# Kernel tuning notes

Hardware: AMD Instinct MI355X
Metric: run time of the kernel (lower is better)

## Reference

```python
import jax, jax.numpy as jnp
import numpy as np

C = 512   # in_channels
N = 256   # spatial side (H == W required by the bmm structure)


def setup_inputs() -> dict:
    key = jax.random.key(0)
    kx, kf, kg, kh = jax.random.split(key, 4)
    scale = 1.0 / np.sqrt(C)  # spectral-normalized 1x1 conv weights have ~unit spectral norm
    x = jax.random.normal(kx, (C, N, N), dtype=jnp.float32)
    Wf = jax.random.normal(kf, (C, C), dtype=jnp.float32) * scale  # 1x1 conv kernel squeezed
    Wg = jax.random.normal(kg, (C, C), dtype=jnp.float32) * scale
    Wh = jax.random.normal(kh, (C, C), dtype=jnp.float32) * scale
    return {"x": x, "Wf": Wf, "Wg": Wg, "Wh": Wh}


def reference(x, Wf, Wg, Wh):
    # 1x1 convs (no bias) == channel-mixing matmuls: out[c,h,w] = sum_k W[c,k] x[k,h,w]
    f = jnp.einsum('ck,khw->chw', Wf, x)
    g = jnp.einsum('ck,khw->chw', Wg, x)
    h = jnp.einsum('ck,khw->chw', Wh, x)
    # torch.bmm(f, g): per-channel HxW @ HxW matmul -> [C, N, N]
    scores = jnp.einsum('cik,ckj->cij', f, g)
    # nn.Softmax(dim=1) on [C, N, N] -> softmax over the row axis (axis=1)
    attn_map = jax.nn.softmax(scores, axis=1)
    # torch.bmm(h, attn_map) -> [C, N, N]
    attn = jnp.einsum('cik,ckj->cij', h, attn_map)
    return x + attn
```

## Files before the change

### kernel.cpp

```cpp
#include <hip/hip_runtime.h>

typedef unsigned short u16;
typedef unsigned int   u32;
typedef __attribute__((ext_vector_type(8))) _Float16 half8;
typedef __attribute__((ext_vector_type(4))) float f32x4;
typedef __attribute__((ext_vector_type(2))) float f32x2;
typedef __attribute__((ext_vector_type(4))) u32   u32x4;
typedef __attribute__((ext_vector_type(4))) unsigned short u16x4;

#define MFMAH __builtin_amdgcn_mfma_f32_16x16x32_f16

__device__ u16 W16[786432];

__device__ __forceinline__ u16 f2h(float f) {
  _Float16 h = (_Float16)f;
  union { _Float16 hh; u16 u; } cv; cv.hh = h; return cv.u;
}
__device__ __forceinline__ u32 pkh(float a, float b) {
  return (u32)f2h(a) | ((u32)f2h(b) << 16);
}
__device__ __forceinline__ void gload16(const void* g, void* l) {
  __builtin_amdgcn_global_load_lds(
      (const __attribute__((address_space(1))) void*)g,
      (__attribute__((address_space(3))) void*)l, 16, 0, 0);
}

__global__ __launch_bounds__(256)
void prep_w(const float* __restrict__ Wf, const float* __restrict__ Wg,
            const float* __restrict__ Wh)
{
  const int r = blockIdx.x;
  const int k = threadIdx.x * 2;
  const float* src = (r < 512) ? (Wf + (size_t)r * 512)
                   : (r < 1024) ? (Wg + (size_t)(r - 512) * 512)
                                : (Wh + (size_t)(r - 1024) * 512);
  f32x2 v = *(const f32x2*)(src + k);
  *(u32*)(W16 + (size_t)r * 512 + k) = pkh(v[0], v[1]);
}

__global__ __launch_bounds__(256)
void prep_x(const float* __restrict__ x, u16* __restrict__ x16)
{
  __shared__ float tile[64 * 256];
  const int bk = blockIdx.x & 7, bn = blockIdx.x >> 3;
  const int t = threadIdx.x;
  const int cw = (t & 63) * 4, r0 = (t >> 6) * 16;
#pragma unroll
  for (int it = 0; it < 16; ++it) {
    const int r = r0 + it;
    *(f32x4*)&tile[r * 256 + cw] =
        *(const f32x4*)(x + (size_t)(bk * 64 + r) * 65536 + (size_t)bn * 256 + cw);
  }
  __syncthreads();
  u32 w[32];
#pragma unroll
  for (int q = 0; q < 32; ++q)
    w[q] = pkh(tile[(2 * q) * 256 + t], tile[(2 * q + 1) * 256 + t]);
  const size_t ob = (size_t)(bn * 256 + t) * 512 + bk * 64;
#pragma unroll
  for (int c4 = 0; c4 < 8; ++c4)
    *(u32x4*)(x16 + ob + c4 * 8) = (u32x4){w[4*c4], w[4*c4+1], w[4*c4+2], w[4*c4+3]};
}

__global__ __launch_bounds__(512, 4)
void conv_fgh(const u16* __restrict__ x16, u16* __restrict__ fb,
              u16* __restrict__ gTb, u16* __restrict__ hb)
{
  __shared__ u16 sA[8192], sB[4096];
  const int bid = blockIdx.x;
  const int xcd = bid & 7, idx = bid >> 3;
  const int tn = xcd * 64 + idx / 6;
  const int tm2 = idx % 6;
  const bool gmode = (tm2 >= 2) && (tm2 < 4);
  const int t = threadIdx.x, lane = t & 63, wid = t >> 6;
  const int wr = wid >> 1, wc = wid & 1, lr = lane & 15, lq = lane >> 4;

  const int ar0 = t >> 2, ar1 = 128 + (t >> 2);
  const int aks0 = (((t & 3) ^ ((ar0 >> 1) & 3)) << 3);
  const int aks1 = (((t & 3) ^ ((ar1 >> 1) & 3)) << 3);
  const int garA0 = tm2 * 256 + ar0, garA1 = tm2 * 256 + ar1;
  const int br = t >> 2;
  const int bks = (((t & 3) ^ ((br >> 1) & 3)) << 3);
  const int bxr = gmode ? ((((tn & 1) << 7) + br) * 256 + (tn >> 1)) : (tn * 128 + br);

  int offA[4], offB[4];
#pragma unroll
  for (int mi = 0; mi < 4; ++mi) {
    const int rowA = wr * 64 + mi * 16 + lr;
    offA[mi] = rowA * 32 + ((lq ^ ((rowA >> 1) & 3)) << 3);
  }
#pragma unroll
  for (int ni = 0; ni < 4; ++ni) {
    const int rowB = wc * 64 + ni * 16 + lr;
    offB[ni] = rowB * 32 + ((lq ^ ((rowB >> 1) & 3)) << 3);
  }

  f32x4 acc[4][4] = {};

  for (int k0 = 0; k0 < 512; k0 += 32) {
    gload16(W16 + (size_t)garA0 * 512 + k0 + aks0, (char*)sA + t * 16);
    gload16(W16 + (size_t)garA1 * 512 + k0 + aks1, (char*)sA + 8192 + t * 16);
    gload16(x16 + (size_t)bxr * 512 + k0 + bks,    (char*)sB + t * 16);
    __syncthreads();
    half8 a[4], b[4];
#pragma unroll
    for (int mi = 0; mi < 4; ++mi) a[mi] = *(const half8*)(sA + offA[mi]);
#pragma unroll
    for (int ni = 0; ni < 4; ++ni) b[ni] = *(const half8*)(sB + offB[ni]);
#pragma unroll
    for (int mi = 0; mi < 4; ++mi)
#pragma unroll
      for (int ni = 0; ni < 4; ++ni)
        acc[mi][ni] = MFMAH(a[mi], b[ni], acc[mi][ni], 0, 0, 0);
    __syncthreads();
  }

  const int cls = tm2 >> 1;
  u16* dst = (cls == 0) ? fb : (cls == 1) ? gTb : hb;
  const int rbase = (tm2 & 1) * 256 + wr * 64;
  const int cbase = tn * 128 + wc * 64;
#pragma unroll
  for (int mi = 0; mi < 4; ++mi)
#pragma unroll
    for (int ni = 0; ni < 4; ++ni) {
      const int r0 = rbase + mi * 16 + lq * 4;
      const int cc = cbase + ni * 16 + lr;
#pragma unroll
      for (int r = 0; r < 4; ++r)
        dst[(size_t)(r0 + r) * 65536 + cc] = f2h(acc[mi][ni][r]);
    }
}

__global__ __launch_bounds__(512)
void scores_kernel(const u16* __restrict__ fb, const u16* __restrict__ gTb,
                   u16* __restrict__ Pt)
{
  __shared__ u16 sA[8192];
  __shared__ u16 sB[4096];
  __shared__ float cmax[512], csum[512];
  const int bid = blockIdx.x;
  const int xcd = bid & 7, i2 = bid >> 3;
  const int c = xcd * 64 + (i2 >> 1), jt = i2 & 1;
  const size_t cb = (size_t)c * 65536;
  const int t = threadIdx.x, lane = t & 63, wid = t >> 6;
  const int wr = wid >> 1, wc = wid & 1, lr = lane & 15, lq = lane >> 4;

  const int arow0 = t >> 2, arow1 = 128 + (t >> 2);
  const int aks0 = (((t & 3) ^ ((arow0 >> 1) & 3)) << 3);
  const int aks1 = (((t & 3) ^ ((arow1 >> 1) & 3)) << 3);
  const int brow = t >> 2;
  const int bks  = (((t & 3) ^ ((brow >> 1) & 3)) << 3);

  int offA[4], offB[4];
#pragma unroll
  for (int mi = 0; mi < 4; ++mi) {
    const int rowA = wr * 64 + mi * 16 + lr;
    offA[mi] = rowA * 32 + ((lq ^ ((rowA >> 1) & 3)) << 3);
  }
#pragma unroll
  for (int ni = 0; ni < 4; ++ni) {
    const int rowB = wc * 64 + ni * 16 + lr;
    offB[ni] = rowB * 32 + ((lq ^ ((rowB >> 1) & 3)) << 3);
  }

  f32x4 acc[4][4] = {};

  for (int k0 = 0; k0 < 256; k0 += 32) {
    gload16(fb + cb + (size_t)arow0 * 256 + k0 + aks0, (char*)sA + t * 16);
    gload16(fb + cb + (size_t)arow1 * 256 + k0 + aks1, (char*)sA + 8192 + t * 16);
    gload16(gTb + cb + (size_t)(jt * 128 + brow) * 256 + k0 + bks, (char*)sB + t * 16);
    __syncthreads();
    half8 a[4], b[4];
#pragma unroll
    for (int mi = 0; mi < 4; ++mi) a[mi] = *(const half8*)(sA + offA[mi]);
#pragma unroll
    for (int ni = 0; ni < 4; ++ni) b[ni] = *(const half8*)(sB + offB[ni]);
#pragma unroll
    for (int mi = 0; mi < 4; ++mi)
#pragma unroll
      for (int ni = 0; ni < 4; ++ni)
        acc[mi][ni] = MFMAH(a[mi], b[ni], acc[mi][ni], 0, 0, 0);
    __syncthreads();
  }

#pragma unroll
  for (int ni = 0; ni < 4; ++ni) {
    const int col = wc * 64 + ni * 16 + lr;
    float m = -3.4e38f;
#pragma unroll
    for (int mi = 0; mi < 4; ++mi) {
      f32x4 a = acc[mi][ni];
      m = fmaxf(m, fmaxf(fmaxf(a[0], a[1]), fmaxf(a[2], a[3])));
    }
    m = fmaxf(m, __shfl_xor(m, 16));
    m = fmaxf(m, __shfl_xor(m, 32));
    cmax[wr * 128 + col] = m;
  }
  __syncthreads();
#pragma unroll
  for (int ni = 0; ni < 4; ++ni) {
    const int col = wc * 64 + ni * 16 + lr;
    const float M = fmaxf(fmaxf(cmax[col], cmax[128 + col]),
                          fmaxf(cmax[256 + col], cmax[384 + col]));
    float s = 0.f;
#pragma unroll
    for (int mi = 0; mi < 4; ++mi)
#pragma unroll
      for (int r = 0; r < 4; ++r) {
        float e = __expf(acc[mi][ni][r] - M);
        acc[mi][ni][r] = e; s += e;
      }
    s += __shfl_xor(s, 16);
    s += __shfl_xor(s, 32);
    csum[wr * 128 + col] = s;
  }
  __syncthreads();
#pragma unroll
  for (int ni = 0; ni < 4; ++ni) {
    const int col = wc * 64 + ni * 16 + lr;
    const float rs = 1.f / (csum[col] + csum[128 + col] + csum[256 + col] + csum[384 + col]);
    const int j = jt * 128 + col;
#pragma unroll
    for (int mi = 0; mi < 4; ++mi) {
      u16x4 w = { f2h(acc[mi][ni][0] * rs), f2h(acc[mi][ni][1] * rs),
                  f2h(acc[mi][ni][2] * rs), f2h(acc[mi][ni][3] * rs) };
      *(u16x4*)(Pt + cb + (size_t)j * 256 + wr * 64 + mi * 16 + lq * 4) = w;
    }
  }
}

__global__ __launch_bounds__(512, 4)
void attn_kernel(const u16* __restrict__ hb, const u16* __restrict__ Pt,
                 const float* __restrict__ x, float* __restrict__ out)
{
  __shared__ u16 sA[8192], sB[4096];
  const int bid = blockIdx.x;
  const int xcd = bid & 7, i2 = bid >> 3;
  const int c = xcd * 64 + (i2 >> 1), tn = i2 & 1;
  const size_t cb = (size_t)c * 65536;
  const int t = threadIdx.x, lane = t & 63, wid = t >> 6;
  const int wr = wid >> 1, wc = wid & 1, lr = lane & 15, lq = lane >> 4;

  const int ar0 = t >> 2, ar1 = 128 + (t >> 2);
  const int aks0 = (((t & 3) ^ ((ar0 >> 1) & 3)) << 3);
  const int aks1 = (((t & 3) ^ ((ar1 >> 1) & 3)) << 3);
  const int br = t >> 2;
  const int bks = (((t & 3) ^ ((br >> 1) & 3)) << 3);

  int offA[4], offB[4];
#pragma unroll
  for (int mi = 0; mi < 4; ++mi) {
    const int rowA = wr * 64 + mi * 16 + lr;
    offA[mi] = rowA * 32 + ((lq ^ ((rowA >> 1) & 3)) << 3);
  }
#pragma unroll
  for (int ni = 0; ni < 4; ++ni) {
    const int rowB = wc * 64 + ni * 16 + lr;
    offB[ni] = rowB * 32 + ((lq ^ ((rowB >> 1) & 3)) << 3);
  }

  f32x4 acc[4][4] = {};

  for (int k0 = 0; k0 < 256; k0 += 32) {
    gload16(hb + cb + (size_t)ar0 * 256 + k0 + aks0, (char*)sA + t * 16);
    gload16(hb + cb + (size_t)ar1 * 256 + k0 + aks1, (char*)sA + 8192 + t * 16);
    gload16(Pt + cb + (size_t)(tn * 128 + br) * 256 + k0 + bks, (char*)sB + t * 16);
    __syncthreads();
    half8 a[4], b[4];
#pragma unroll
    for (int mi = 0; mi < 4; ++mi) a[mi] = *(const half8*)(sA + offA[mi]);
#pragma unroll
    for (int ni = 0; ni < 4; ++ni) b[ni] = *(const half8*)(sB + offB[ni]);
#pragma unroll
    for (int mi = 0; mi < 4; ++mi)
#pragma unroll
      for (int ni = 0; ni < 4; ++ni)
        acc[mi][ni] = MFMAH(a[mi], b[ni], acc[mi][ni], 0, 0, 0);
    __syncthreads();
  }

  const float* Xc = x + cb;
  float* Oc = out + cb;
  const int rbase = wr * 64;
  const int cbase = tn * 128 + wc * 64;
#pragma unroll
  for (int mi = 0; mi < 4; ++mi)
#pragma unroll
    for (int ni = 0; ni < 4; ++ni) {
      const int r0 = rbase + mi * 16 + lq * 4, cc = cbase + ni * 16 + lr;
#pragma unroll
      for (int r = 0; r < 4; ++r) {
        const size_t idx = (size_t)(r0 + r) * 256 + cc;
        Oc[idx] = Xc[idx] + acc[mi][ni][r];
      }
    }
}

extern "C" void kernel_launch(void* const* d_in, const int* in_sizes, int n_in,
                              void* d_out, int out_size, void* d_ws, size_t ws_size,
                              hipStream_t stream)
{
  (void)in_sizes; (void)n_in; (void)out_size; (void)ws_size;
  const float* x  = (const float*)d_in[0];
  const float* Wf = (const float*)d_in[1];
  const float* Wg = (const float*)d_in[2];
  const float* Wh = (const float*)d_in[3];
  float* out = (float*)d_out;
  char*  ws  = (char*)d_ws;

  u16* x16  = (u16*)ws;
  u16* gT16 = (u16*)(ws + 67108864);
  u16* h16  = (u16*)(ws + 134217728);
  u16* f16  = (u16*)d_out;
  u16* Pt   = x16;

  dim3 blk(256, 1, 1);
  prep_w       <<<dim3(1536, 1, 1), blk, 0, stream>>>(Wf, Wg, Wh);
  prep_x       <<<dim3(2048, 1, 1), blk, 0, stream>>>(x, x16);
  conv_fgh     <<<dim3(3072, 1, 1), dim3(512, 1, 1), 0, stream>>>(x16, f16, gT16, h16);
  scores_kernel<<<dim3(1024, 1, 1), dim3(512, 1, 1), 0, stream>>>(f16, gT16, Pt);
  attn_kernel  <<<dim3(1024, 1, 1), dim3(512, 1, 1), 0, stream>>>(h16, Pt, x, out);
}
```

Before: 354.8 us.

## Keep weight tile resident in LDS and loop over pixel tiles in conv kernel

The 1x1-conv kernel now loads a 128x512 fp16 weight slab into LDS once per block and then iterates over 8 pixel tiles of 128 columns, streaming x16 with a double-buffered K loop. This replaces the 3072-block grid that reloaded weight tiles every K step with 768 persistent-ish blocks, cutting redundant weight traffic and LDS staging. It costs much larger LDS use (144KB), lower occupancy (launch bounds 2), and a smaller per-wave N tile (64x32).

```diff
diff --git a/kernel.cpp b/kernel.cpp
--- a/kernel.cpp
+++ b/kernel.cpp
@@ -62,73 +62,92 @@
     *(u32x4*)(x16 + ob + c4 * 8) = (u32x4){w[4*c4], w[4*c4+1], w[4*c4+2], w[4*c4+3]};
 }
 
-__global__ __launch_bounds__(512, 4)
+__global__ __launch_bounds__(512, 2)
 void conv_fgh(const u16* __restrict__ x16, u16* __restrict__ fb,
               u16* __restrict__ gTb, u16* __restrict__ hb)
 {
-  __shared__ u16 sA[8192], sB[4096];
+  __shared__ u16 lds[73728];
+  char* const L = (char*)lds;
   const int bid = blockIdx.x;
   const int xcd = bid & 7, idx = bid >> 3;
-  const int tn = xcd * 64 + idx / 6;
-  const int tm2 = idx % 6;
-  const bool gmode = (tm2 >= 2) && (tm2 < 4);
+  const int p = xcd * 8 + idx / 12;
+  const int s = idx % 12;
+  const int cls = s >> 2, mloc = s & 3;
+  const bool gmode = (cls == 1);
   const int t = threadIdx.x, lane = t & 63, wid = t >> 6;
-  const int wr = wid >> 1, wc = wid & 1, lr = lane & 15, lq = lane >> 4;
-
-  const int ar0 = t >> 2, ar1 = 128 + (t >> 2);
-  const int aks0 = (((t & 3) ^ ((ar0 >> 1) & 3)) << 3);
-  const int aks1 = (((t & 3) ^ ((ar1 >> 1) & 3)) << 3);
-  const int garA0 = tm2 * 256 + ar0, garA1 = tm2 * 256 + ar1;
-  const int br = t >> 2;
-  const int bks = (((t & 3) ^ ((br >> 1) & 3)) << 3);
-  const int bxr = gmode ? ((((tn & 1) << 7) + br) * 256 + (tn >> 1)) : (tn * 128 + br);
-
-  int offA[4], offB[4];
+  const int wr = wid >> 2, wc = wid & 3, lr = lane & 15, lq = lane >> 4;
+
+#pragma unroll
+  for (int q = 0; q < 16; ++q) {
+    const int r = q * 8 + wid;
+    const int wrow = cls * 512 + mloc * 128 + r;
+    const int k = ((lane ^ (r & 7)) << 3);
+    gload16(W16 + (size_t)wrow * 512 + k, L + r * 1024 + lane * 16);
+  }
+
+  const int bcol = t >> 2, bslot = t & 3;
+  const int bko = ((bslot ^ ((bcol >> 1) & 3)) << 3);
+
+  int offArow[4], rowA7[4];
 #pragma unroll
   for (int mi = 0; mi < 4; ++mi) {
     const int rowA = wr * 64 + mi * 16 + lr;
-    offA[mi] = rowA * 32 + ((lq ^ ((rowA >> 1) & 3)) << 3);
-  }
-#pragma unroll
-  for (int ni = 0; ni < 4; ++ni) {
-    const int rowB = wc * 64 + ni * 16 + lr;
-    offB[ni] = rowB * 32 + ((lq ^ ((rowB >> 1) & 3)) << 3);
-  }
-
-  f32x4 acc[4][4] = {};
-
-  for (int k0 = 0; k0 < 512; k0 += 32) {
-    gload16(W16 + (size_t)garA0 * 512 + k0 + aks0, (char*)sA + t * 16);
-    gload16(W16 + (size_t)garA1 * 512 + k0 + aks1, (char*)sA + 8192 + t * 16);
-    gload16(x16 + (size_t)bxr * 512 + k0 + bks,    (char*)sB + t * 16);
-    __syncthreads();
-    half8 a[4], b[4];
-#pragma unroll
-    for (int mi = 0; mi < 4; ++mi) a[mi] = *(const half8*)(sA + offA[mi]);
-#pragma unroll
-    for (int ni = 0; ni < 4; ++ni) b[ni] = *(const half8*)(sB + offB[ni]);
+    offArow[mi] = rowA * 1024;
+    rowA7[mi] = rowA & 7;
+  }
+  int offB[2];
+#pragma unroll
+  for (int ni = 0; ni < 2; ++ni) {
+    const int colB = wc * 32 + ni * 16 + lr;
+    offB[ni] = 131072 + colB * 64 + ((lq ^ ((colB >> 1) & 3)) << 4);
+  }
+
+  __syncthreads();
+
+#pragma unroll 1
+  for (int pi = 0; pi < 8; ++pi) {
+    const int jg = p * 1024 + pi * 128 + bcol;
+    const size_t bxr = gmode ? ((size_t)(jg & 255) * 256 + (jg >> 8)) : (size_t)jg;
+    gload16(x16 + bxr * 512 + bko, L + 131072 + t * 16);
+    __syncthreads();
+
+    f32x4 acc[4][2] = {};
+#pragma unroll 1
+    for (int T = 0; T < 16; ++T) {
+      if (T < 15)
+        gload16(x16 + bxr * 512 + (T + 1) * 32 + bko,
+                L + 131072 + ((T + 1) & 1) * 8192 + t * 16);
+      const int bb = (T & 1) << 13;
+      const int t4 = T * 4;
+      half8 a[4], b[2];
+#pragma unroll
+      for (int mi = 0; mi < 4; ++mi)
+        a[mi] = *(const half8*)(L + offArow[mi] + (((t4 + lq) ^ rowA7[mi]) << 4));
+#pragma unroll
+      for (int ni = 0; ni < 2; ++ni)
+        b[ni] = *(const half8*)(L + offB[ni] + bb);
+#pragma unroll
+      for (int mi = 0; mi < 4; ++mi)
+#pragma unroll
+        for (int ni = 0; ni < 2; ++ni)
+          acc[mi][ni] = MFMAH(a[mi], b[ni], acc[mi][ni], 0, 0, 0);
+      __syncthreads();
+    }
+
+    u16* dst = (cls == 0) ? fb : (cls == 1) ? gTb : hb;
+    const int rbase = mloc * 128 + wr * 64;
+    const int cb0 = p * 1024 + pi * 128 + wc * 32;
 #pragma unroll
     for (int mi = 0; mi < 4; ++mi)
 #pragma unroll
-      for (int ni = 0; ni < 4; ++ni)
-        acc[mi][ni] = MFMAH(a[mi], b[ni], acc[mi][ni], 0, 0, 0);
-    __syncthreads();
-  }
-
-  const int cls = tm2 >> 1;
-  u16* dst = (cls == 0) ? fb : (cls == 1) ? gTb : hb;
-  const int rbase = (tm2 & 1) * 256 + wr * 64;
-  const int cbase = tn * 128 + wc * 64;
-#pragma unroll
-  for (int mi = 0; mi < 4; ++mi)
-#pragma unroll
-    for (int ni = 0; ni < 4; ++ni) {
-      const int r0 = rbase + mi * 16 + lq * 4;
-      const int cc = cbase + ni * 16 + lr;
-#pragma unroll
-      for (int r = 0; r < 4; ++r)
-        dst[(size_t)(r0 + r) * 65536 + cc] = f2h(acc[mi][ni][r]);
-    }
+      for (int ni = 0; ni < 2; ++ni) {
+        const int r0 = rbase + mi * 16 + lq * 4;
+        const int cc = cb0 + ni * 16 + lr;
+#pragma unroll
+        for (int r = 0; r < 4; ++r)
+          dst[(size_t)(r0 + r) * 65536 + cc] = f2h(acc[mi][ni][r]);
+      }
+  }
 }
 
 __global__ __launch_bounds__(512)
@@ -317,7 +336,7 @@
   dim3 blk(256, 1, 1);
   prep_w       <<<dim3(1536, 1, 1), blk, 0, stream>>>(Wf, Wg, Wh);
   prep_x       <<<dim3(2048, 1, 1), blk, 0, stream>>>(x, x16);
-  conv_fgh     <<<dim3(3072, 1, 1), dim3(512, 1, 1), 0, stream>>>(x16, f16, gT16, h16);
+  conv_fgh     <<<dim3(768, 1, 1), dim3(512, 1, 1), 0, stream>>>(x16, f16, gT16, h16);
   scores_kernel<<<dim3(1024, 1, 1), dim3(512, 1, 1), 0, stream>>>(f16, gT16, Pt);
   attn_kernel  <<<dim3(1024, 1, 1), dim3(512, 1, 1), 0, stream>>>(h16, Pt, x, out);
 }
```

Result: slower. 374.2 us (+5.5%).

## Retile conv_fgh to 128x128 tiles with 256 threads and K-step 64

Applied to the files above, without the earlier changes.

The 1x1-conv GEMM kernel drops from 512-thread blocks computing 256x128 output tiles to 256-thread blocks computing 128x128 tiles. It now stages 64-wide K slices instead of 32-wide ones, with an 8-way XOR swizzle on the shared-memory layout, and launches twice as many blocks. The goal is to halve the number of barrier-separated load/compute iterations and to improve occupancy and scheduling granularity. In exchange, each block reuses its weight tile less, so more global traffic goes to the W loads.

```diff
diff --git a/kernel.cpp b/kernel.cpp
--- a/kernel.cpp
+++ b/kernel.cpp
@@ -62,62 +62,72 @@
     *(u32x4*)(x16 + ob + c4 * 8) = (u32x4){w[4*c4], w[4*c4+1], w[4*c4+2], w[4*c4+3]};
 }
 
-__global__ __launch_bounds__(512, 4)
+__global__ __launch_bounds__(256)
 void conv_fgh(const u16* __restrict__ x16, u16* __restrict__ fb,
               u16* __restrict__ gTb, u16* __restrict__ hb)
 {
-  __shared__ u16 sA[8192], sB[4096];
+  __shared__ u16 sA[8192], sB[8192];
   const int bid = blockIdx.x;
   const int xcd = bid & 7, idx = bid >> 3;
-  const int tn = xcd * 64 + idx / 6;
-  const int tm2 = idx % 6;
-  const bool gmode = (tm2 >= 2) && (tm2 < 4);
+  const int tn = xcd * 64 + idx / 12;
+  const int tm = idx % 12;
+  const bool gmode = (tm >= 4) && (tm < 8);
   const int t = threadIdx.x, lane = t & 63, wid = t >> 6;
   const int wr = wid >> 1, wc = wid & 1, lr = lane & 15, lq = lane >> 4;
 
-  const int ar0 = t >> 2, ar1 = 128 + (t >> 2);
-  const int aks0 = (((t & 3) ^ ((ar0 >> 1) & 3)) << 3);
-  const int aks1 = (((t & 3) ^ ((ar1 >> 1) & 3)) << 3);
-  const int garA0 = tm2 * 256 + ar0, garA1 = tm2 * 256 + ar1;
-  const int br = t >> 2;
-  const int bks = (((t & 3) ^ ((br >> 1) & 3)) << 3);
-  const int bxr = gmode ? ((((tn & 1) << 7) + br) * 256 + (tn >> 1)) : (tn * 128 + br);
-
-  int offA[4], offB[4];
+  const int srow = t >> 3, sslot = t & 7;
+  int arow_g[4]; size_t bxr_g[4]; int ksw[4];
+#pragma unroll
+  for (int q = 0; q < 4; ++q) {
+    const int row = q * 32 + srow;
+    ksw[q] = ((sslot ^ (row & 7)) << 3);
+    arow_g[q] = tm * 128 + row;
+    const int jg = tn * 128 + row;
+    bxr_g[q] = gmode ? ((size_t)(jg & 255) * 256 + (jg >> 8)) : (size_t)jg;
+  }
+
+  int offA[4], a7[4], offB[4], b7[4];
 #pragma unroll
   for (int mi = 0; mi < 4; ++mi) {
     const int rowA = wr * 64 + mi * 16 + lr;
-    offA[mi] = rowA * 32 + ((lq ^ ((rowA >> 1) & 3)) << 3);
+    offA[mi] = rowA * 64; a7[mi] = rowA & 7;
   }
 #pragma unroll
   for (int ni = 0; ni < 4; ++ni) {
     const int rowB = wc * 64 + ni * 16 + lr;
-    offB[ni] = rowB * 32 + ((lq ^ ((rowB >> 1) & 3)) << 3);
+    offB[ni] = rowB * 64; b7[ni] = rowB & 7;
   }
 
   f32x4 acc[4][4] = {};
 
-  for (int k0 = 0; k0 < 512; k0 += 32) {
-    gload16(W16 + (size_t)garA0 * 512 + k0 + aks0, (char*)sA + t * 16);
-    gload16(W16 + (size_t)garA1 * 512 + k0 + aks1, (char*)sA + 8192 + t * 16);
-    gload16(x16 + (size_t)bxr * 512 + k0 + bks,    (char*)sB + t * 16);
-    __syncthreads();
-    half8 a[4], b[4];
-#pragma unroll
-    for (int mi = 0; mi < 4; ++mi) a[mi] = *(const half8*)(sA + offA[mi]);
-#pragma unroll
-    for (int ni = 0; ni < 4; ++ni) b[ni] = *(const half8*)(sB + offB[ni]);
-#pragma unroll
-    for (int mi = 0; mi < 4; ++mi)
+  for (int k0 = 0; k0 < 512; k0 += 64) {
+#pragma unroll
+    for (int q = 0; q < 4; ++q) {
+      gload16(W16 + (size_t)arow_g[q] * 512 + k0 + ksw[q], (char*)sA + q * 4096 + t * 16);
+      gload16(x16 + bxr_g[q] * 512 + k0 + ksw[q],          (char*)sB + q * 4096 + t * 16);
+    }
+    __syncthreads();
+#pragma unroll
+    for (int kk = 0; kk < 2; ++kk) {
+      half8 a[4], b[4];
+#pragma unroll
+      for (int mi = 0; mi < 4; ++mi)
+        a[mi] = *(const half8*)(sA + offA[mi] + (((kk * 4 + lq) ^ a7[mi]) << 3));
 #pragma unroll
       for (int ni = 0; ni < 4; ++ni)
-        acc[mi][ni] = MFMAH(a[mi], b[ni], acc[mi][ni], 0, 0, 0);
-    __syncthreads();
-  }
-
-  const int cls = tm2 >> 1;
+        b[ni] = *(const half8*)(sB + offB[ni] + (((kk * 4 + lq) ^ b7[ni]) << 3));
+#pragma unroll
+      for (int mi = 0; mi < 4; ++mi)
+#pragma unroll
+        for (int ni = 0; ni < 4; ++ni)
+          acc[mi][ni] = MFMAH(a[mi], b[ni], acc[mi][ni], 0, 0, 0);
+    }
+    __syncthreads();
+  }
+
+  const int cls = tm >> 2;
   u16* dst = (cls == 0) ? fb : (cls == 1) ? gTb : hb;
-  const int rbase = (tm2 & 1) * 256 + wr * 64;
+  const int rbase = (tm & 3) * 128 + wr * 64;
   const int cbase = tn * 128 + wc * 64;
 #pragma unroll
   for (int mi = 0; mi < 4; ++mi)
@@ -317,7 +327,7 @@
   dim3 blk(256, 1, 1);
   prep_w       <<<dim3(1536, 1, 1), blk, 0, stream>>>(Wf, Wg, Wh);
   prep_x       <<<dim3(2048, 1, 1), blk, 0, stream>>>(x, x16);
-  conv_fgh     <<<dim3(3072, 1, 1), dim3(512, 1, 1), 0, stream>>>(x16, f16, gT16, h16);
+  conv_fgh     <<<dim3(6144, 1, 1), blk, 0, stream>>>(x16, f16, gT16, h16);
   scores_kernel<<<dim3(1024, 1, 1), dim3(512, 1, 1), 0, stream>>>(f16, gT16, Pt);
   attn_kernel  <<<dim3(1024, 1, 1), dim3(512, 1, 1), 0, stream>>>(h16, Pt, x, out);
 }
```

Measured after the change: 357.3 us. Within noise of the previous version (+0.7%).
